# Optimization experiments

Hardware: AMD Instinct MI355X
Metric: run time of the kernel (lower is better)

The kernel has to match this reference:

```python
import jax, jax.numpy as jnp
import numpy as np

N = 100000      # nodes
E = 1600000     # directed edges (avg degree 16)
F_IN = 512      # config.input_layer
H1, D1 = 8, 8   # conv1: 8 heads x 8 dims
C_OUT = 40      # config.output_layer


def setup_inputs() -> dict:
    key = jax.random.key(0)
    ks = jax.random.split(key, 10)
    x = jax.random.normal(ks[0], (N, F_IN), dtype=jnp.float32)
    edge_index = jax.random.randint(ks[1], (2, E), 0, N, dtype=jnp.int64)
    s = 0.05
    W1 = jax.random.normal(ks[2], (F_IN, H1 * D1), dtype=jnp.float32) * s
    att_src1 = jax.random.normal(ks[3], (H1, D1), dtype=jnp.float32) * s
    att_dst1 = jax.random.normal(ks[4], (H1, D1), dtype=jnp.float32) * s
    b1 = jnp.zeros((H1 * D1,), dtype=jnp.float32)
    W2 = jax.random.normal(ks[5], (H1 * D1, C_OUT), dtype=jnp.float32) * s
    att_src2 = jax.random.normal(ks[6], (1, C_OUT), dtype=jnp.float32) * s
    att_dst2 = jax.random.normal(ks[7], (1, C_OUT), dtype=jnp.float32) * s
    b2 = jnp.zeros((C_OUT,), dtype=jnp.float32)
    return {"x": x, "edge_index": edge_index,
            "W1": W1, "att_src1": att_src1, "att_dst1": att_dst1, "b1": b1,
            "W2": W2, "att_src2": att_src2, "att_dst2": att_dst2, "b2": b2}


def _gat_conv(x, src, dst, W, a_src, a_dst, b, heads, concat):
    """PyG GATConv (eval mode: attention dropout is identity)."""
    n = x.shape[0]
    d = W.shape[1] // heads
    h = (x @ W).reshape(n, heads, d)                       # [N,H,D]
    alpha_s = jnp.einsum('nhd,hd->nh', h, a_src)           # [N,H]
    alpha_d = jnp.einsum('nhd,hd->nh', h, a_dst)
    e = jax.nn.leaky_relu(alpha_s[src] + alpha_d[dst], 0.2)  # [E,H]
    # numerically stable segment softmax over edges grouped by dst
    e = e - jax.ops.segment_max(e, dst, num_segments=n)[dst]
    ex = jnp.exp(e)
    denom = jax.ops.segment_sum(ex, dst, num_segments=n)[dst]
    alpha = ex / denom                                      # [E,H]
    msg = h[src] * alpha[:, :, None]                        # [E,H,D]
    out = jax.ops.segment_sum(msg, dst, num_segments=n)     # [N,H,D]
    out = out.reshape(n, heads * d) if concat else out.mean(axis=1)
    return out + b


def reference(x, edge_index, W1, att_src1, att_dst1, b1, W2, att_src2, att_dst2, b2):
    # add self loops (PyG GATConv default)
    loop = jnp.arange(x.shape[0], dtype=edge_index.dtype)
    src = jnp.concatenate([edge_index[0], loop])
    dst = jnp.concatenate([edge_index[1], loop])
    # dropout(p=0.6) layers are identity in eval mode
    h = jax.nn.elu(_gat_conv(x, src, dst, W1, att_src1, att_dst1, b1, H1, True))
    out = _gat_conv(h, src, dst, W2, att_src2, att_dst2, b2, 1, False)
    return jax.nn.log_softmax(out, axis=1)
```

## Files before the change

kernel.cpp:

```cpp
#include <hip/hip_runtime.h>

#define F_IN 512
#define H1   8
#define D1   8
#define C1   64
#define C2   40
#define C2P  48

#define BKT_SH   7
#define BKT_W    128
#define NBKT_MAX 1024
#define NBLK     128

using short8 = __attribute__((ext_vector_type(8))) short;
using f32x4  = __attribute__((ext_vector_type(4))) float;
using bf8v   = __attribute__((ext_vector_type(8))) __bf16;

__device__ __forceinline__ float leaky02(float x) { return x > 0.f ? x : 0.2f * x; }
__device__ __forceinline__ float bf2f(unsigned short u) {
    return __builtin_bit_cast(float, ((unsigned)u) << 16);
}
__device__ __forceinline__ unsigned short f2bf(float v) {
    return __builtin_bit_cast(unsigned short, (__bf16)v);
}
__device__ __forceinline__ short8 cvt_bf16x8(float4 a, float4 b) {
    bf8v r;
    r[0] = (__bf16)a.x; r[1] = (__bf16)a.y; r[2] = (__bf16)a.z; r[3] = (__bf16)a.w;
    r[4] = (__bf16)b.x; r[5] = (__bf16)b.y; r[6] = (__bf16)b.z; r[7] = (__bf16)b.w;
    return __builtin_bit_cast(short8, r);
}

__global__ __launch_bounds__(256) void wconv_kernel(
    const float* __restrict__ W1, const float* __restrict__ W2,
    unsigned short* __restrict__ Bt1, unsigned short* __restrict__ Bt2)
{
    int idx = blockIdx.x * 256 + threadIdx.x;
    if (idx < F_IN * C1) {
        int k = idx >> 6, c = idx & 63;
        Bt1[(size_t)c * F_IN + k] = f2bf(W1[idx]);
    } else if (idx < F_IN * C1 + C2P * 64) {
        int j = idx - F_IN * C1;
        int c = j >> 6, k = j & 63;
        float v = (c < C2) ? W2[k * C2 + c] : 0.f;
        Bt2[c * 64 + k] = f2bf(v);
    }
}

__global__ __launch_bounds__(256) void fused1_kernel(
    const float* __restrict__ x, const unsigned short* __restrict__ Bt1,
    const float* __restrict__ a_src, const float* __restrict__ a_dst,
    unsigned short* __restrict__ h1b, float* __restrict__ as1,
    float* __restrict__ ad1, int N,
    const int* __restrict__ ei, int* __restrict__ blockhist,
    int E, int nbkt, int chunk, int G1)
{
    __shared__ int lh[NBKT_MAX];
    const int blk = blockIdx.x;
    const int tid = threadIdx.x;

    if (blk >= G1) {
        const int b = blk - G1;
        for (int i = tid; i < nbkt; i += 256) lh[i] = 0;
        __syncthreads();
        const int beg = b * chunk;
        const int end = min(E, beg + chunk);
        for (int e = beg + tid; e < end; e += 256)
            atomicAdd(&lh[ei[E + e] >> BKT_SH], 1);
        __syncthreads();
        for (int k = tid; k < nbkt; k += 256)
            blockhist[k * NBLK + b] = lh[k];
        return;
    }

    const int w    = tid >> 6;
    const int lane = tid & 63;
    const int lo   = lane & 15;
    const int kg   = lane >> 4;
    const int n0   = blk * 128 + w * 32;

    const int nA = min(n0 + lo, N - 1);
    const int nB = min(n0 + 16 + lo, N - 1);
    const float* xA = x + (size_t)nA * F_IN + kg * 8;
    const float* xB = x + (size_t)nB * F_IN + kg * 8;
    const unsigned short* bp = Bt1 + (size_t)lo * F_IN + kg * 8;

    float a_s[4], a_d[4];
    #pragma unroll
    for (int nt = 0; nt < 4; ++nt) {
        a_s[nt] = a_src[nt * 16 + lo];
        a_d[nt] = a_dst[nt * 16 + lo];
    }

    f32x4 acc[2][4];
    #pragma unroll
    for (int mt = 0; mt < 2; ++mt)
        #pragma unroll
        for (int nt = 0; nt < 4; ++nt)
            acc[mt][nt] = (f32x4){0.f, 0.f, 0.f, 0.f};

    #pragma unroll 4
    for (int s = 0; s < 16; ++s) {
        const int kb = s * 32;
        float4 a0 = *(const float4*)(xA + kb);
        float4 a1 = *(const float4*)(xA + kb + 4);
        float4 c0 = *(const float4*)(xB + kb);
        float4 c1 = *(const float4*)(xB + kb + 4);
        short8 bF[4];
        #pragma unroll
        for (int nt = 0; nt < 4; ++nt)
            bF[nt] = *(const short8*)(bp + (size_t)nt * 16 * F_IN + kb);
        short8 aF0 = cvt_bf16x8(a0, a1);
        short8 aF1 = cvt_bf16x8(c0, c1);
        #pragma unroll
        for (int nt = 0; nt < 4; ++nt) {
            acc[0][nt] = __builtin_amdgcn_mfma_f32_16x16x32_bf16(aF0, bF[nt], acc[0][nt], 0, 0, 0);
            acc[1][nt] = __builtin_amdgcn_mfma_f32_16x16x32_bf16(aF1, bF[nt], acc[1][nt], 0, 0, 0);
        }
    }

    #pragma unroll
    for (int mt = 0; mt < 2; ++mt) {
        #pragma unroll
        for (int j = 0; j < 4; ++j) {
            const int n = n0 + mt * 16 + kg * 4 + j;
            float sv[4], dv[4];
            #pragma unroll
            for (int nt = 0; nt < 4; ++nt) {
                float v = acc[mt][nt][j];
                sv[nt] = v * a_s[nt];
                dv[nt] = v * a_d[nt];
            }
            #pragma unroll
            for (int m = 1; m < 8; m <<= 1) {
                #pragma unroll
                for (int nt = 0; nt < 4; ++nt) {
                    sv[nt] += __shfl_xor(sv[nt], m);
                    dv[nt] += __shfl_xor(dv[nt], m);
                }
            }
            if (n < N) {
                #pragma unroll
                for (int nt = 0; nt < 4; ++nt)
                    h1b[(size_t)n * C1 + nt * 16 + lo] = f2bf(acc[mt][nt][j]);
                if ((lane & 7) == 0) {
                    const int h0 = (lane >> 3) & 1;
                    #pragma unroll
                    for (int nt = 0; nt < 4; ++nt) {
                        as1[n * H1 + h0 + nt * 2] = sv[nt];
                        ad1[n * H1 + h0 + nt * 2] = dv[nt];
                    }
                }
            }
        }
    }
}

__global__ __launch_bounds__(512) void scan1_kernel(
    const int* __restrict__ in, int* __restrict__ excl,
    int* __restrict__ bsum, int M)
{
    __shared__ int sA[512], sB[512];
    const int t = threadIdx.x;
    const int i = blockIdx.x * 512 + t;
    int v = (i < M) ? in[i] : 0;
    sA[t] = v; __syncthreads();
    int* pin = sA; int* pout = sB;
    #pragma unroll
    for (int off = 1; off < 512; off <<= 1) {
        pout[t] = pin[t] + ((t >= off) ? pin[t - off] : 0);
        __syncthreads();
        int* tmp = pin; pin = pout; pout = tmp;
    }
    if (i < M) excl[i] = pin[t] - v;
    if (t == 511) bsum[blockIdx.x] = pin[511];
}

__global__ __launch_bounds__(256) void scan2_kernel(
    int* __restrict__ bsum, int* __restrict__ bsumo, int NB)
{
    __shared__ int sA[256], sB[256];
    const int t = threadIdx.x;
    int v = (t < NB) ? bsum[t] : 0;
    sA[t] = v; __syncthreads();
    int* pin = sA; int* pout = sB;
    #pragma unroll
    for (int off = 1; off < 256; off <<= 1) {
        pout[t] = pin[t] + ((t >= off) ? pin[t - off] : 0);
        __syncthreads();
        int* tmp = pin; pin = pout; pout = tmp;
    }
    if (t < NB) bsumo[t] = pin[t] - v;
}

__global__ __launch_bounds__(256) void bpart_kernel(
    const int* __restrict__ ei, const int* __restrict__ boffs,
    const int* __restrict__ bsumo, int* __restrict__ ebuf,
    int E, int nbkt, int chunk)
{
    __shared__ int cur[NBKT_MAX];
    const int b = blockIdx.x;
    for (int k = threadIdx.x; k < nbkt; k += 256) {
        const int idx = k * NBLK + b;
        cur[k] = boffs[idx] + bsumo[idx >> 9];
    }
    __syncthreads();
    const int beg = b * chunk;
    const int end = min(E, beg + chunk);
    for (int e = beg + threadIdx.x; e < end; e += 256) {
        int src = ei[e], dst = ei[E + e];
        int pos = atomicAdd(&cur[dst >> BKT_SH], 1);
        ebuf[pos] = (src << BKT_SH) | (dst & (BKT_W - 1));
    }
}

__global__ __launch_bounds__(256) void bsort_kernel(
    const int* __restrict__ boffs, const int* __restrict__ bsumo,
    const int* __restrict__ ebuf, int* __restrict__ rowptr,
    int* __restrict__ esrc, int N, int E, int nbkt)
{
    const int b = blockIdx.x;
    const int tid = threadIdx.x;
    const int i0 = b * NBLK;
    const int base = boffs[i0] + bsumo[i0 >> 9];
    int nxt;
    if (b == nbkt - 1) nxt = E;
    else {
        const int i1 = (b + 1) * NBLK;
        nxt = boffs[i1] + bsumo[i1 >> 9];
    }
    const int cnt = nxt - base;

    __shared__ int hist[BKT_W], scn[BKT_W], cur[BKT_W];
    if (tid < BKT_W) hist[tid] = 0;
    __syncthreads();
    for (int i = tid; i < cnt; i += 256)
        atomicAdd(&hist[ebuf[base + i] & (BKT_W - 1)], 1);
    __syncthreads();
    if (tid < BKT_W) scn[tid] = hist[tid];
    __syncthreads();
    #pragma unroll
    for (int off = 1; off < BKT_W; off <<= 1) {
        int add = 0;
        if (tid < BKT_W && tid >= off) add = scn[tid - off];
        __syncthreads();
        if (tid < BKT_W) scn[tid] += add;
        __syncthreads();
    }
    if (tid < BKT_W) {
        int ex = base + scn[tid] - hist[tid];
        cur[tid] = ex;
        int n0 = b * BKT_W + tid;
        if (n0 < N) rowptr[n0] = ex;
    }
    if (b == 0 && tid == 0) rowptr[N] = E;
    __syncthreads();
    for (int i = tid; i < cnt; i += 256) {
        int p = ebuf[base + i];
        int pos = atomicAdd(&cur[p & (BKT_W - 1)], 1);
        esrc[pos] = (unsigned)p >> BKT_SH;
    }
}

__global__ __launch_bounds__(256) void agg1_kernel(
    const int* __restrict__ rowptr, const int* __restrict__ esrc,
    const unsigned short* __restrict__ h1b, const float* __restrict__ as1,
    const float* __restrict__ ad1, const float* __restrict__ b1,
    unsigned short* __restrict__ h1f, int N)
{
    const int n = blockIdx.x * 4 + (threadIdx.x >> 6);
    if (n >= N) return;
    const int lane = threadIdx.x & 63;
    const int h = lane >> 3;
    const float adh = ad1[n * H1 + h];

    float acc = 0.f, den = 0.f;
    int i = rowptr[n];
    const int end = rowptr[n + 1];
    for (; i + 4 <= end; i += 4) {
        const int s0 = esrc[i], s1 = esrc[i + 1], s2 = esrc[i + 2], s3 = esrc[i + 3];
        const float v0 = bf2f(h1b[(size_t)s0 * C1 + lane]);
        const float v1 = bf2f(h1b[(size_t)s1 * C1 + lane]);
        const float v2 = bf2f(h1b[(size_t)s2 * C1 + lane]);
        const float v3 = bf2f(h1b[(size_t)s3 * C1 + lane]);
        const float a0 = as1[s0 * H1 + h], a1 = as1[s1 * H1 + h];
        const float a2 = as1[s2 * H1 + h], a3 = as1[s3 * H1 + h];
        const float e0 = __expf(leaky02(a0 + adh));
        const float e1 = __expf(leaky02(a1 + adh));
        const float e2 = __expf(leaky02(a2 + adh));
        const float e3 = __expf(leaky02(a3 + adh));
        acc += e0 * v0; acc += e1 * v1; acc += e2 * v2; acc += e3 * v3;
        den += (e0 + e1) + (e2 + e3);
    }
    for (; i < end; ++i) {
        const int src = esrc[i];
        const float v  = bf2f(h1b[(size_t)src * C1 + lane]);
        const float ex = __expf(leaky02(as1[src * H1 + h] + adh));
        acc += ex * v;
        den += ex;
    }
    {
        const float ex = __expf(leaky02(as1[n * H1 + h] + adh));
        acc += ex * bf2f(h1b[(size_t)n * C1 + lane]);
        den += ex;
    }
    float v = acc / den + b1[lane];
    v = v > 0.f ? v : __expf(v) - 1.f;
    h1f[(size_t)n * C1 + lane] = f2bf(v);
}

__global__ __launch_bounds__(256) void gemm2_kernel(
    const unsigned short* __restrict__ h1f, const unsigned short* __restrict__ Bt2,
    const float* __restrict__ a_src2, const float* __restrict__ a_dst2,
    unsigned short* __restrict__ h2b, float* __restrict__ as2,
    float* __restrict__ ad2, int N)
{
    const int tid  = threadIdx.x;
    const int w    = tid >> 6;
    const int lane = tid & 63;
    const int lo   = lane & 15;
    const int kg   = lane >> 4;
    const int n0   = blockIdx.x * 64 + w * 16;

    const int nA = min(n0 + lo, N - 1);
    const unsigned short* ap = h1f + (size_t)nA * C1 + kg * 8;

    float a_s[3], a_d[3];
    #pragma unroll
    for (int nt = 0; nt < 3; ++nt) {
        const int c = nt * 16 + lo;
        a_s[nt] = (c < C2) ? a_src2[c] : 0.f;
        a_d[nt] = (c < C2) ? a_dst2[c] : 0.f;
    }

    f32x4 acc[3];
    #pragma unroll
    for (int nt = 0; nt < 3; ++nt) acc[nt] = (f32x4){0.f, 0.f, 0.f, 0.f};

    #pragma unroll
    for (int ks = 0; ks < 2; ++ks) {
        short8 aF = *(const short8*)(ap + ks * 32);
        #pragma unroll
        for (int nt = 0; nt < 3; ++nt) {
            short8 bF = *(const short8*)(Bt2 + (nt * 16 + lo) * 64 + ks * 32 + kg * 8);
            acc[nt] = __builtin_amdgcn_mfma_f32_16x16x32_bf16(aF, bF, acc[nt], 0, 0, 0);
        }
    }

    #pragma unroll
    for (int j = 0; j < 4; ++j) {
        const int n = n0 + kg * 4 + j;
        float s = acc[0][j] * a_s[0] + acc[1][j] * a_s[1] + acc[2][j] * a_s[2];
        float d = acc[0][j] * a_d[0] + acc[1][j] * a_d[1] + acc[2][j] * a_d[2];
        #pragma unroll
        for (int m = 1; m < 16; m <<= 1) {
            s += __shfl_xor(s, m);
            d += __shfl_xor(d, m);
        }
        if (n < N) {
            #pragma unroll
            for (int nt = 0; nt < 3; ++nt) {
                const int c = nt * 16 + lo;
                if (c < C2) h2b[(size_t)n * C2 + c] = f2bf(acc[nt][j]);
            }
            if (lo == 0) { as2[n] = s; ad2[n] = d; }
        }
    }
}

__global__ __launch_bounds__(256) void agg2_kernel(
    const int* __restrict__ rowptr, const int* __restrict__ esrc,
    const unsigned short* __restrict__ h2b, const float* __restrict__ as2,
    const float* __restrict__ ad2, const float* __restrict__ b2,
    float* __restrict__ out, int N)
{
    const int n = blockIdx.x * 4 + (threadIdx.x >> 6);
    if (n >= N) return;
    const int lane = threadIdx.x & 63;
    const float adn = ad2[n];

    float acc = 0.f, den = 0.f;
    int i = rowptr[n];
    const int end = rowptr[n + 1];
    for (; i + 4 <= end; i += 4) {
        const int s0 = esrc[i], s1 = esrc[i + 1], s2 = esrc[i + 2], s3 = esrc[i + 3];
        float v0 = 0.f, v1 = 0.f, v2 = 0.f, v3 = 0.f;
        if (lane < C2) {
            v0 = bf2f(h2b[(size_t)s0 * C2 + lane]);
            v1 = bf2f(h2b[(size_t)s1 * C2 + lane]);
            v2 = bf2f(h2b[(size_t)s2 * C2 + lane]);
            v3 = bf2f(h2b[(size_t)s3 * C2 + lane]);
        }
        const float a0 = as2[s0], a1 = as2[s1], a2 = as2[s2], a3 = as2[s3];
        const float e0 = __expf(leaky02(a0 + adn));
        const float e1 = __expf(leaky02(a1 + adn));
        const float e2 = __expf(leaky02(a2 + adn));
        const float e3 = __expf(leaky02(a3 + adn));
        acc += e0 * v0; acc += e1 * v1; acc += e2 * v2; acc += e3 * v3;
        den += (e0 + e1) + (e2 + e3);
    }
    for (; i < end; ++i) {
        const int src = esrc[i];
        float v = (lane < C2) ? bf2f(h2b[(size_t)src * C2 + lane]) : 0.f;
        const float ex = __expf(leaky02(as2[src] + adn));
        acc += ex * v;
        den += ex;
    }
    {
        const float ex = __expf(leaky02(as2[n] + adn));
        if (lane < C2) acc += ex * bf2f(h2b[(size_t)n * C2 + lane]);
        den += ex;
    }
    float v = (lane < C2) ? (acc / den + b2[lane]) : -1e30f;
    float m = v;
    #pragma unroll
    for (int s = 1; s < 64; s <<= 1) m = fmaxf(m, __shfl_xor(m, s));
    float e2x = (lane < C2) ? __expf(v - m) : 0.f;
    #pragma unroll
    for (int s = 1; s < 64; s <<= 1) e2x += __shfl_xor(e2x, s);
    float lse = __logf(e2x);
    if (lane < C2) out[(size_t)n * C2 + lane] = v - m - lse;
}

extern "C" void kernel_launch(void* const* d_in, const int* in_sizes, int n_in,
                              void* d_out, int out_size, void* d_ws, size_t ws_size,
                              hipStream_t stream)
{
    const float* x    = (const float*)d_in[0];
    const int*   ei   = (const int*)  d_in[1];
    const float* W1   = (const float*)d_in[2];
    const float* as1w = (const float*)d_in[3];
    const float* ad1w = (const float*)d_in[4];
    const float* b1   = (const float*)d_in[5];
    const float* W2   = (const float*)d_in[6];
    const float* as2w = (const float*)d_in[7];
    const float* ad2w = (const float*)d_in[8];
    const float* b2   = (const float*)d_in[9];

    const int N = in_sizes[0] / F_IN;
    const int E = in_sizes[1] / 2;
    const int nbkt = (N + BKT_W - 1) >> BKT_SH;
    const int M    = nbkt * NBLK;
    const int chunk = (E + NBLK - 1) / NBLK;
    const int G1   = (N + 127) / 128;

    char* base = (char*)d_ws;
    auto carve = [&](size_t bytes) -> void* {
        void* p = (void*)base;
        base += (bytes + 255) & ~(size_t)255;
        return p;
    };
    unsigned short* h1b = (unsigned short*)carve((size_t)N * C1 * 2);
    unsigned short* h1f = (unsigned short*)carve((size_t)N * C1 * 2);
    float* as1    = (float*)carve((size_t)N * H1 * 4);
    float* ad1    = (float*)carve((size_t)N * H1 * 4);
    unsigned short* h2b = (unsigned short*)carve((size_t)N * C2 * 2);
    float* as2    = (float*)carve((size_t)N * 4);
    float* ad2    = (float*)carve((size_t)N * 4);
    int*   rowptr = (int*)carve((size_t)(N + 1) * 4);
    int*   esrc   = (int*)carve((size_t)E * 4);
    int*   boffs  = (int*)carve((size_t)(M + 1) * 4);
    int*   bsum   = (int*)carve(256 * 4);
    int*   bsumo  = (int*)carve(256 * 4);
    unsigned short* Bt1 = (unsigned short*)carve((size_t)F_IN * C1 * 2);
    unsigned short* Bt2 = (unsigned short*)carve((size_t)C2P * 64 * 2);

    int* ebuf = (int*)h1f;

    const int NB = (M + 511) / 512;

    wconv_kernel<<<(F_IN * C1 + C2P * 64 + 255) / 256, 256, 0, stream>>>(W1, W2, Bt1, Bt2);

    fused1_kernel<<<G1 + NBLK, 256, 0, stream>>>(
        x, Bt1, as1w, ad1w, h1b, as1, ad1, N, ei, boffs, E, nbkt, chunk, G1);

    scan1_kernel<<<NB, 512, 0, stream>>>(boffs, boffs, bsum, M);
    scan2_kernel<<<1, 256, 0, stream>>>(bsum, bsumo, NB);
    bpart_kernel<<<NBLK, 256, 0, stream>>>(ei, boffs, bsumo, ebuf, E, nbkt, chunk);
    bsort_kernel<<<nbkt, 256, 0, stream>>>(boffs, bsumo, ebuf, rowptr, esrc, N, E, nbkt);

    agg1_kernel<<<(N + 3) / 4, 256, 0, stream>>>(rowptr, esrc, h1b, as1, ad1, b1, h1f, N);
    gemm2_kernel<<<(N + 63) / 64, 256, 0, stream>>>(h1f, Bt2, as2w, ad2w, h2b, as2, ad2, N);
    agg2_kernel<<<(N + 3) / 4, 256, 0, stream>>>(rowptr, esrc, h2b, as2, ad2, b2,
                                                 (float*)d_out, N);
}
```

Measured before the change: 313.0 us.

## Split layer-1 GEMM across the three CSR-build kernels to overlap work

The layer-1 GEMM blocks were all co-scheduled with the histogram kernel. They are now split into three portions (1/4, 3/8, rest), each appended to the histogram, partition and bucket-sort kernels. The aim is to hide the small, latency-bound CSR construction phases behind dense GEMM work. It adds extra blocks to each sort kernel, which can delay their completion, and the split ratios are fixed.

```diff
diff --git a/kernel.cpp b/kernel.cpp
--- a/kernel.cpp
+++ b/kernel.cpp
@@ -46,37 +46,18 @@
     }
 }
 
-__global__ __launch_bounds__(256) void fused1_kernel(
+__device__ __forceinline__ void gemm1_body(
+    int gblk, int tid,
     const float* __restrict__ x, const unsigned short* __restrict__ Bt1,
     const float* __restrict__ a_src, const float* __restrict__ a_dst,
     unsigned short* __restrict__ h1b, float* __restrict__ as1,
-    float* __restrict__ ad1, int N,
-    const int* __restrict__ ei, int* __restrict__ blockhist,
-    int E, int nbkt, int chunk, int G1)
-{
-    __shared__ int lh[NBKT_MAX];
-    const int blk = blockIdx.x;
-    const int tid = threadIdx.x;
-
-    if (blk >= G1) {
-        const int b = blk - G1;
-        for (int i = tid; i < nbkt; i += 256) lh[i] = 0;
-        __syncthreads();
-        const int beg = b * chunk;
-        const int end = min(E, beg + chunk);
-        for (int e = beg + tid; e < end; e += 256)
-            atomicAdd(&lh[ei[E + e] >> BKT_SH], 1);
-        __syncthreads();
-        for (int k = tid; k < nbkt; k += 256)
-            blockhist[k * NBLK + b] = lh[k];
-        return;
-    }
-
+    float* __restrict__ ad1, int N)
+{
     const int w    = tid >> 6;
     const int lane = tid & 63;
     const int lo   = lane & 15;
     const int kg   = lane >> 4;
-    const int n0   = blk * 128 + w * 32;
+    const int n0   = gblk * 128 + w * 32;
 
     const int nA = min(n0 + lo, N - 1);
     const int nB = min(n0 + 16 + lo, N - 1);
@@ -155,6 +136,33 @@
     }
 }
 
+__global__ __launch_bounds__(256) void fusedA_kernel(
+    const int* __restrict__ ei, int* __restrict__ blockhist,
+    int E, int nbkt, int chunk,
+    const float* __restrict__ x, const unsigned short* __restrict__ Bt1,
+    const float* __restrict__ a_src, const float* __restrict__ a_dst,
+    unsigned short* __restrict__ h1b, float* __restrict__ as1,
+    float* __restrict__ ad1, int N, int g1_beg)
+{
+    __shared__ int lh[NBKT_MAX];
+    const int blk = blockIdx.x;
+    const int tid = threadIdx.x;
+    if (blk < NBLK) {
+        const int b = blk;
+        for (int i = tid; i < nbkt; i += 256) lh[i] = 0;
+        __syncthreads();
+        const int beg = b * chunk;
+        const int end = min(E, beg + chunk);
+        for (int e = beg + tid; e < end; e += 256)
+            atomicAdd(&lh[ei[E + e] >> BKT_SH], 1);
+        __syncthreads();
+        for (int k = tid; k < nbkt; k += 256)
+            blockhist[k * NBLK + b] = lh[k];
+        return;
+    }
+    gemm1_body(g1_beg + blk - NBLK, tid, x, Bt1, a_src, a_dst, h1b, as1, ad1, N);
+}
+
 __global__ __launch_bounds__(512) void scan1_kernel(
     const int* __restrict__ in, int* __restrict__ excl,
     int* __restrict__ bsum, int M)
@@ -192,73 +200,92 @@
     if (t < NB) bsumo[t] = pin[t] - v;
 }
 
-__global__ __launch_bounds__(256) void bpart_kernel(
+__global__ __launch_bounds__(256) void fusedB_kernel(
     const int* __restrict__ ei, const int* __restrict__ boffs,
     const int* __restrict__ bsumo, int* __restrict__ ebuf,
-    int E, int nbkt, int chunk)
+    int E, int nbkt, int chunk,
+    const float* __restrict__ x, const unsigned short* __restrict__ Bt1,
+    const float* __restrict__ a_src, const float* __restrict__ a_dst,
+    unsigned short* __restrict__ h1b, float* __restrict__ as1,
+    float* __restrict__ ad1, int N, int g1_beg)
 {
     __shared__ int cur[NBKT_MAX];
-    const int b = blockIdx.x;
-    for (int k = threadIdx.x; k < nbkt; k += 256) {
-        const int idx = k * NBLK + b;
-        cur[k] = boffs[idx] + bsumo[idx >> 9];
-    }
-    __syncthreads();
-    const int beg = b * chunk;
-    const int end = min(E, beg + chunk);
-    for (int e = beg + threadIdx.x; e < end; e += 256) {
-        int src = ei[e], dst = ei[E + e];
-        int pos = atomicAdd(&cur[dst >> BKT_SH], 1);
-        ebuf[pos] = (src << BKT_SH) | (dst & (BKT_W - 1));
-    }
-}
-
-__global__ __launch_bounds__(256) void bsort_kernel(
+    const int blk = blockIdx.x;
+    const int tid = threadIdx.x;
+    if (blk < NBLK) {
+        const int b = blk;
+        for (int k = tid; k < nbkt; k += 256) {
+            const int idx = k * NBLK + b;
+            cur[k] = boffs[idx] + bsumo[idx >> 9];
+        }
+        __syncthreads();
+        const int beg = b * chunk;
+        const int end = min(E, beg + chunk);
+        for (int e = beg + tid; e < end; e += 256) {
+            int src = ei[e], dst = ei[E + e];
+            int pos = atomicAdd(&cur[dst >> BKT_SH], 1);
+            ebuf[pos] = (src << BKT_SH) | (dst & (BKT_W - 1));
+        }
+        return;
+    }
+    gemm1_body(g1_beg + blk - NBLK, tid, x, Bt1, a_src, a_dst, h1b, as1, ad1, N);
+}
+
+__global__ __launch_bounds__(256) void fusedC_kernel(
     const int* __restrict__ boffs, const int* __restrict__ bsumo,
     const int* __restrict__ ebuf, int* __restrict__ rowptr,
-    int* __restrict__ esrc, int N, int E, int nbkt)
-{
-    const int b = blockIdx.x;
+    int* __restrict__ esrc, int N, int E, int nbkt,
+    const float* __restrict__ x, const unsigned short* __restrict__ Bt1,
+    const float* __restrict__ a_src, const float* __restrict__ a_dst,
+    unsigned short* __restrict__ h1b, float* __restrict__ as1,
+    float* __restrict__ ad1, int g1_beg)
+{
+    __shared__ int hist[BKT_W], scn[BKT_W], cur[BKT_W];
+    const int blk = blockIdx.x;
     const int tid = threadIdx.x;
-    const int i0 = b * NBLK;
-    const int base = boffs[i0] + bsumo[i0 >> 9];
-    int nxt;
-    if (b == nbkt - 1) nxt = E;
-    else {
-        const int i1 = (b + 1) * NBLK;
-        nxt = boffs[i1] + bsumo[i1 >> 9];
-    }
-    const int cnt = nxt - base;
-
-    __shared__ int hist[BKT_W], scn[BKT_W], cur[BKT_W];
-    if (tid < BKT_W) hist[tid] = 0;
-    __syncthreads();
-    for (int i = tid; i < cnt; i += 256)
-        atomicAdd(&hist[ebuf[base + i] & (BKT_W - 1)], 1);
-    __syncthreads();
-    if (tid < BKT_W) scn[tid] = hist[tid];
-    __syncthreads();
-    #pragma unroll
-    for (int off = 1; off < BKT_W; off <<= 1) {
-        int add = 0;
-        if (tid < BKT_W && tid >= off) add = scn[tid - off];
-        __syncthreads();
-        if (tid < BKT_W) scn[tid] += add;
-        __syncthreads();
-    }
-    if (tid < BKT_W) {
-        int ex = base + scn[tid] - hist[tid];
-        cur[tid] = ex;
-        int n0 = b * BKT_W + tid;
-        if (n0 < N) rowptr[n0] = ex;
-    }
-    if (b == 0 && tid == 0) rowptr[N] = E;
-    __syncthreads();
-    for (int i = tid; i < cnt; i += 256) {
-        int p = ebuf[base + i];
-        int pos = atomicAdd(&cur[p & (BKT_W - 1)], 1);
-        esrc[pos] = (unsigned)p >> BKT_SH;
-    }
+    if (blk < nbkt) {
+        const int b = blk;
+        const int i0 = b * NBLK;
+        const int base = boffs[i0] + bsumo[i0 >> 9];
+        int nxt;
+        if (b == nbkt - 1) nxt = E;
+        else {
+            const int i1 = (b + 1) * NBLK;
+            nxt = boffs[i1] + bsumo[i1 >> 9];
+        }
+        const int cnt = nxt - base;
+
+        if (tid < BKT_W) hist[tid] = 0;
+        __syncthreads();
+        for (int i = tid; i < cnt; i += 256)
+            atomicAdd(&hist[ebuf[base + i] & (BKT_W - 1)], 1);
+        __syncthreads();
+        if (tid < BKT_W) scn[tid] = hist[tid];
+        __syncthreads();
+        #pragma unroll
+        for (int off = 1; off < BKT_W; off <<= 1) {
+            int add = 0;
+            if (tid < BKT_W && tid >= off) add = scn[tid - off];
+            __syncthreads();
+            if (tid < BKT_W) scn[tid] += add;
+            __syncthreads();
+        }
+        if (tid < BKT_W) {
+            int ex = base + scn[tid] - hist[tid];
+            cur[tid] = ex;
+            int n0 = b * BKT_W + tid;
+            if (n0 < N) rowptr[n0] = ex;
+        }
+        if (b == 0 && tid == 0) rowptr[N] = E;
+        __syncthreads();
+        for (int i = tid; i < cnt; i += 256) {
+            int p = ebuf[base + i];
+            int pos = atomicAdd(&cur[p & (BKT_W - 1)], 1);
+            esrc[pos] = (unsigned)p >> BKT_SH;
+        }
+        return;
+    }
+    gemm1_body(g1_beg + blk - nbkt, tid, x, Bt1, a_src, a_dst, h1b, as1, ad1, N);
 }
 
 __global__ __launch_bounds__(256) void agg1_kernel(
@@ -442,6 +469,10 @@
     const int M    = nbkt * NBLK;
     const int chunk = (E + NBLK - 1) / NBLK;
     const int G1   = (N + 127) / 128;
+
+    const int CA = G1 / 4;
+    const int CB = (G1 * 3) / 8;
+    const int CC = G1 - CA - CB;
 
     char* base = (char*)d_ws;
     auto carve = [&](size_t bytes) -> void* {
@@ -470,13 +501,20 @@
 
     wconv_kernel<<<(F_IN * C1 + C2P * 64 + 255) / 256, 256, 0, stream>>>(W1, W2, Bt1, Bt2);
 
-    fused1_kernel<<<G1 + NBLK, 256, 0, stream>>>(
-        x, Bt1, as1w, ad1w, h1b, as1, ad1, N, ei, boffs, E, nbkt, chunk, G1);
+    fusedA_kernel<<<NBLK + CA, 256, 0, stream>>>(
+        ei, boffs, E, nbkt, chunk,
+        x, Bt1, as1w, ad1w, h1b, as1, ad1, N, 0);
 
     scan1_kernel<<<NB, 512, 0, stream>>>(boffs, boffs, bsum, M);
     scan2_kernel<<<1, 256, 0, stream>>>(bsum, bsumo, NB);
-    bpart_kernel<<<NBLK, 256, 0, stream>>>(ei, boffs, bsumo, ebuf, E, nbkt, chunk);
-    bsort_kernel<<<nbkt, 256, 0, stream>>>(boffs, bsumo, ebuf, rowptr, esrc, N, E, nbkt);
+
+    fusedB_kernel<<<NBLK + CB, 256, 0, stream>>>(
+        ei, boffs, bsumo, ebuf, E, nbkt, chunk,
+        x, Bt1, as1w, ad1w, h1b, as1, ad1, N, CA);
+
+    fusedC_kernel<<<nbkt + CC, 256, 0, stream>>>(
+        boffs, bsumo, ebuf, rowptr, esrc, N, E, nbkt,
+        x, Bt1, as1w, ad1w, h1b, as1, ad1, CA + CB);
 
     agg1_kernel<<<(N + 3) / 4, 256, 0, stream>>>(rowptr, esrc, h1b, as1, ad1, b1, h1f, N);
     gemm2_kernel<<<(N + 63) / 64, 256, 0, stream>>>(h1f, Bt2, as2w, ad2w, h2b, as2, ad2, N);
```

Measured after the change: 320.8 us. 1.02x slower.
